# Performance work log

Hardware: AMD Instinct MI355X
Metric: run time of the kernel (lower is better)

The kernel has to match this reference:

```python
import jax, jax.numpy as jnp
import numpy as np

N = 20000
E = 320000
IN = 256
H = 4
C = 64
NEG_SLOPE = 0.2


def setup_inputs() -> dict:
    key = jax.random.key(0)
    ks = jax.random.split(key, 12)
    HC = H * C

    def w(k, shape, fan_in):
        return jax.random.normal(k, shape, dtype=jnp.float32) / np.sqrt(fan_in)

    x = jax.random.normal(ks[0], (N, IN), dtype=jnp.float32)
    edge_index = jax.random.randint(ks[1], (2, E), 0, N, dtype=jnp.int64)
    return {
        "x": x,
        "edge_index": edge_index,
        "Wl1": w(ks[2], (IN, HC), IN),
        "Wr1": w(ks[3], (IN, HC), IN),
        "att1": w(ks[4], (H, C), C),
        "b1": jnp.zeros((HC,), dtype=jnp.float32),
        "Wl2": w(ks[5], (HC, HC), HC),
        "Wr2": w(ks[6], (HC, HC), HC),
        "att2": w(ks[7], (H, C), C),
        "b2": jnp.zeros((HC,), dtype=jnp.float32),
        "Wfc": w(ks[8], (HC, 2), HC),
        "bfc": jnp.zeros((2,), dtype=jnp.float32),
    }


def _gatv2(x, src, dst, Wl, Wr, att, b):
    """GATv2Conv (concat=True, share_weights=False), inference (no dropout)."""
    n = x.shape[0]
    xl = (x @ Wl).reshape(n, H, C)  # source-side projection
    xr = (x @ Wr).reshape(n, H, C)  # target-side projection
    # per-edge GATv2 score: a^T LeakyReLU(xl_j + xr_i)
    e = jax.nn.leaky_relu(xl[src] + xr[dst], NEG_SLOPE)      # [E, H, C]
    score = jnp.einsum("ehc,hc->eh", e, att)                 # [E, H]
    # segment softmax over incoming edges of each target node
    smax = jax.ops.segment_max(score, dst, num_segments=n)   # [N, H]
    ex = jnp.exp(score - smax[dst])
    denom = jax.ops.segment_sum(ex, dst, num_segments=n)     # [N, H]
    alpha = ex / denom[dst]                                  # [E, H]
    # scatter-aggregate messages (source projections weighted by alpha)
    out = jax.ops.segment_sum(alpha[:, :, None] * xl[src], dst, num_segments=n)
    return out.reshape(n, H * C) + b


def reference(x, edge_index, Wl1, Wr1, att1, b1, Wl2, Wr2, att2, b2, Wfc, bfc):
    n = x.shape[0]
    # add_self_loops=True (PyG default)
    loop = jnp.arange(n, dtype=edge_index.dtype)
    src = jnp.concatenate([edge_index[0], loop])
    dst = jnp.concatenate([edge_index[1], loop])

    h = _gatv2(x, src, dst, Wl1, Wr1, att1, b1)
    h = jax.nn.relu(h)
    h = _gatv2(h, src, dst, Wl2, Wr2, att2, b2)
    h = jax.nn.relu(h)
    g = jnp.mean(h, axis=0, keepdims=True)  # [1, H*C]
    return g @ Wfc + bfc                    # [1, 2]
```

## Files before the change

### kernel.cpp

```cpp
#include <hip/hip_runtime.h>
#include <hip/hip_bf16.h>
#include <math.h>

#define Nn 20000
#define Ee 320000
#define INF_ 256
#define Hh 4
#define Cc 64
#define HC 256
#define NB_ 79
#define NEG_SLOPE 0.2f

using frag16 = __attribute__((ext_vector_type(8))) short;
using f32x4  = __attribute__((ext_vector_type(4))) float;

__device__ __forceinline__ void async16(const void* g, void* l) {
    __builtin_amdgcn_global_load_lds(
        (const __attribute__((address_space(1))) unsigned int*)g,
        (__attribute__((address_space(3))) unsigned int*)l,
        16, 0, 0);
}


__global__ void hist_kernel(const int* __restrict__ dst, int ne, int* deg) {
    int e = blockIdx.x * blockDim.x + threadIdx.x;
    if (e < ne) atomicAdd(&deg[dst[e]], 1);
}

#define SCAN_PER 20
__global__ __launch_bounds__(1024) void scan_all(const int* __restrict__ deg,
                                                 int* __restrict__ row_start,
                                                 int* __restrict__ cursor) {
    int tid = threadIdx.x;
    int lane = tid & 63, w = tid >> 6;
    int base = tid * SCAN_PER;
    int local[SCAN_PER];
    int sum = 0;
    #pragma unroll
    for (int i = 0; i < SCAN_PER; ++i) {
        int idx = base + i;
        int v = (idx < Nn) ? deg[idx] : 0;
        local[i] = sum;
        sum += v;
    }
    int x = sum;
    #pragma unroll
    for (int off = 1; off < 64; off <<= 1) {
        int y = __shfl_up(x, off, 64);
        if (lane >= off) x += y;
    }
    __shared__ int wsum[16];
    if (lane == 63) wsum[w] = x;
    __syncthreads();
    int wadd = 0;
    for (int k = 0; k < w; ++k) wadd += wsum[k];
    int texcl = (x - sum) + wadd;
    #pragma unroll
    for (int i = 0; i < SCAN_PER; ++i) {
        int idx = base + i;
        if (idx < Nn) {
            int v = texcl + local[i];
            row_start[idx] = v;
            cursor[idx] = v;
        }
    }
    if (tid == 1023) row_start[Nn] = texcl + sum;
}

__global__ void scatter_kernel(const int* __restrict__ src, const int* __restrict__ dst,
                               int ne, int n, int* cursor, int* colx) {
    int e = blockIdx.x * blockDim.x + threadIdx.x;
    if (e < ne) {
        int d = dst[e];
        int pos = atomicAdd(&cursor[d], 1);
        colx[pos] = src[e];
    } else if (e < ne + n) {
        int node = e - ne;
        int pos = atomicAdd(&cursor[node], 1);
        colx[pos] = node;
    }
}


__device__ inline unsigned short bf16rn(float f) {
    unsigned u = __float_as_uint(f);
    unsigned r = (u + 0x7FFFu + ((u >> 16) & 1u)) >> 16;
    return (unsigned short)r;
}

__device__ inline void split1(float v, short& h, short& l) {
    unsigned short hh = bf16rn(v);
    float back = __uint_as_float(((unsigned)hh) << 16);
    unsigned short ll = bf16rn(v - back);
    h = (short)hh; l = (short)ll;
}

__device__ __forceinline__ float4 bf4_to_f4(ushort4 u) {
    return make_float4(__uint_as_float((unsigned)u.x << 16),
                       __uint_as_float((unsigned)u.y << 16),
                       __uint_as_float((unsigned)u.z << 16),
                       __uint_as_float((unsigned)u.w << 16));
}


__global__ __launch_bounds__(256) void prep(const float* __restrict__ x,
                                            const float* __restrict__ Wl1,
                                            const float* __restrict__ Wr1,
                                            const float* __restrict__ Wl2,
                                            const float* __restrict__ Wr2,
                                            short* __restrict__ Ah,
                                            short* __restrict__ Al,
                                            short* __restrict__ WhT1,
                                            short* __restrict__ WlT1,
                                            short* __restrict__ WhT2,
                                            short* __restrict__ WlT2,
                                            int* __restrict__ deg,
                                            float* __restrict__ gpart,
                                            int n4) {
    __shared__ float T[64][65];
    int b = blockIdx.x, tid = threadIdx.x;
    if (b < 64) {
        int m  = b >> 4;
        int tr = (b >> 2) & 3;
        int tc = b & 3;
        const float* W = (m == 0) ? Wl1 : (m == 1) ? Wr1 : (m == 2) ? Wl2 : Wr2;
        short* Wh = (m < 2) ? WhT1 : WhT2;
        short* Wl = (m < 2) ? WlT1 : WlT2;
        int colofs = (m & 1) * 256;
        int lr = tid >> 4;
        int lq = (tid & 15) * 4;
        #pragma unroll
        for (int it = 0; it < 4; ++it) {
            int r = it * 16 + lr;
            float4 v = *(const float4*)&W[(size_t)(tr * 64 + r) * 256 + tc * 64 + lq];
            T[r][lq + 0] = v.x; T[r][lq + 1] = v.y;
            T[r][lq + 2] = v.z; T[r][lq + 3] = v.w;
        }
        __syncthreads();
        #pragma unroll
        for (int it = 0; it < 4; ++it) {
            int cl = it * 16 + lr;
            int kl = (tid & 15) * 4;
            short4 h, l;
            split1(T[kl + 0][cl], h.x, l.x);
            split1(T[kl + 1][cl], h.y, l.y);
            split1(T[kl + 2][cl], h.z, l.z);
            split1(T[kl + 3][cl], h.w, l.w);
            size_t o = (size_t)(colofs + tc * 64 + cl) * 256 + tr * 64 + kl;
            *(short4*)&Wh[o] = h;
            *(short4*)&Wl[o] = l;
        }
    } else {
        int i = (b - 64) * 256 + tid;
        if (i < Nn) deg[i] = 1;
        if (i < 32 * 256) gpart[i] = 0.f;
        if (i < n4) {
            float4 v = ((const float4*)x)[i];
            short4 h, l;
            split1(v.x, h.x, l.x);
            split1(v.y, h.y, l.y);
            split1(v.z, h.z, l.z);
            split1(v.w, h.w, l.w);
            ((short4*)Ah)[i] = h;
            ((short4*)Al)[i] = l;
        }
    }
}


__global__ __launch_bounds__(256, 4) void mfma_gemm(const short* __restrict__ Ah,
                                                    const short* __restrict__ Al,
                                                    const short* __restrict__ WhT,
                                                    const short* __restrict__ WlT,
                                                    unsigned short* __restrict__ XLh,
                                                    float* __restrict__ XR) {
    __shared__ short BsH[64 * 256];
    __shared__ short BsL[64 * 256];

    int tid = threadIdx.x;
    int wave = tid >> 6, lane = tid & 63;
    int quad = lane >> 4, lc = lane & 15;

    int v = blockIdx.x;
    int p = (v & 7) * 79 + (v >> 3);
    int j = p >> 3;
    int colg = p & 7;
    int cbase = (colg * 64) & 255;

    {
        int cl0 = wave * 2 + (lane >> 5);
        int kcs = (lane & 31) ^ (cl0 & 7);
        const short* srcH = WhT + (size_t)(colg * 64 + cl0) * HC + kcs * 8;
        const short* srcL = WlT + (size_t)(colg * 64 + cl0) * HC + kcs * 8;
        short* dstH = &BsH[wave * 512];
        short* dstL = &BsL[wave * 512];
        #pragma unroll
        for (int r = 0; r < 8; ++r) {
            async16(srcH + (size_t)r * 8 * HC, dstH + r * 2048);
            async16(srcL + (size_t)r * 8 * HC, dstL + r * 2048);
        }
    }
    __syncthreads();

    #pragma unroll
    for (int tt = 0; tt < 2; ++tt) {
        int rowt = j + tt * 79;
        if (rowt > 156) break;
        int bm = rowt * 128;

        int row0 = bm + wave * 32 + lc;
        int row1 = row0 + 16;
        int ca0 = (row0 < Nn) ? row0 : (Nn - 1);
        int ca1 = (row1 < Nn) ? row1 : (Nn - 1);
        const short* pa0h = Ah + (size_t)ca0 * HC + quad * 8;
        const short* pa1h = Ah + (size_t)ca1 * HC + quad * 8;
        const short* pa0l = Al + (size_t)ca0 * HC + quad * 8;
        const short* pa1l = Al + (size_t)ca1 * HC + quad * 8;

        f32x4 acc[2][4] = {};
        #pragma unroll
        for (int c = 0; c < 8; ++c) {
            int k0 = c * 32;
            frag16 a0h = *(const frag16*)(pa0h + k0);
            frag16 a1h = *(const frag16*)(pa1h + k0);
            frag16 a0l = *(const frag16*)(pa0l + k0);
            frag16 a1l = *(const frag16*)(pa1l + k0);
            int sw = ((c * 4 + quad) ^ (lc & 7)) * 8;
            frag16 bh0 = *(const frag16*)&BsH[(0 * 16 + lc) * HC + sw];
            frag16 bh1 = *(const frag16*)&BsH[(1 * 16 + lc) * HC + sw];
            frag16 bh2 = *(const frag16*)&BsH[(2 * 16 + lc) * HC + sw];
            frag16 bh3 = *(const frag16*)&BsH[(3 * 16 + lc) * HC + sw];
            frag16 bl0 = *(const frag16*)&BsL[(0 * 16 + lc) * HC + sw];
            frag16 bl1 = *(const frag16*)&BsL[(1 * 16 + lc) * HC + sw];
            frag16 bl2 = *(const frag16*)&BsL[(2 * 16 + lc) * HC + sw];
            frag16 bl3 = *(const frag16*)&BsL[(3 * 16 + lc) * HC + sw];
            acc[0][0] = __builtin_amdgcn_mfma_f32_16x16x32_bf16(bh0, a0h, acc[0][0], 0, 0, 0);
            acc[1][0] = __builtin_amdgcn_mfma_f32_16x16x32_bf16(bh0, a1h, acc[1][0], 0, 0, 0);
            acc[0][1] = __builtin_amdgcn_mfma_f32_16x16x32_bf16(bh1, a0h, acc[0][1], 0, 0, 0);
            acc[1][1] = __builtin_amdgcn_mfma_f32_16x16x32_bf16(bh1, a1h, acc[1][1], 0, 0, 0);
            acc[0][2] = __builtin_amdgcn_mfma_f32_16x16x32_bf16(bh2, a0h, acc[0][2], 0, 0, 0);
            acc[1][2] = __builtin_amdgcn_mfma_f32_16x16x32_bf16(bh2, a1h, acc[1][2], 0, 0, 0);
            acc[0][3] = __builtin_amdgcn_mfma_f32_16x16x32_bf16(bh3, a0h, acc[0][3], 0, 0, 0);
            acc[1][3] = __builtin_amdgcn_mfma_f32_16x16x32_bf16(bh3, a1h, acc[1][3], 0, 0, 0);
            acc[0][0] = __builtin_amdgcn_mfma_f32_16x16x32_bf16(bh0, a0l, acc[0][0], 0, 0, 0);
            acc[1][0] = __builtin_amdgcn_mfma_f32_16x16x32_bf16(bh0, a1l, acc[1][0], 0, 0, 0);
            acc[0][1] = __builtin_amdgcn_mfma_f32_16x16x32_bf16(bh1, a0l, acc[0][1], 0, 0, 0);
            acc[1][1] = __builtin_amdgcn_mfma_f32_16x16x32_bf16(bh1, a1l, acc[1][1], 0, 0, 0);
            acc[0][2] = __builtin_amdgcn_mfma_f32_16x16x32_bf16(bh2, a0l, acc[0][2], 0, 0, 0);
            acc[1][2] = __builtin_amdgcn_mfma_f32_16x16x32_bf16(bh2, a1l, acc[1][2], 0, 0, 0);
            acc[0][3] = __builtin_amdgcn_mfma_f32_16x16x32_bf16(bh3, a0l, acc[0][3], 0, 0, 0);
            acc[1][3] = __builtin_amdgcn_mfma_f32_16x16x32_bf16(bh3, a1l, acc[1][3], 0, 0, 0);
            acc[0][0] = __builtin_amdgcn_mfma_f32_16x16x32_bf16(bl0, a0h, acc[0][0], 0, 0, 0);
            acc[1][0] = __builtin_amdgcn_mfma_f32_16x16x32_bf16(bl0, a1h, acc[1][0], 0, 0, 0);
            acc[0][1] = __builtin_amdgcn_mfma_f32_16x16x32_bf16(bl1, a0h, acc[0][1], 0, 0, 0);
            acc[1][1] = __builtin_amdgcn_mfma_f32_16x16x32_bf16(bl1, a1h, acc[1][1], 0, 0, 0);
            acc[0][2] = __builtin_amdgcn_mfma_f32_16x16x32_bf16(bl2, a0h, acc[0][2], 0, 0, 0);
            acc[1][2] = __builtin_amdgcn_mfma_f32_16x16x32_bf16(bl2, a1h, acc[1][2], 0, 0, 0);
            acc[0][3] = __builtin_amdgcn_mfma_f32_16x16x32_bf16(bl3, a0h, acc[0][3], 0, 0, 0);
            acc[1][3] = __builtin_amdgcn_mfma_f32_16x16x32_bf16(bl3, a1h, acc[1][3], 0, 0, 0);
        }

        #pragma unroll
        for (int mt = 0; mt < 2; ++mt) {
            int rw = bm + wave * 32 + mt * 16 + lc;
            if (rw >= Nn) continue;
            #pragma unroll
            for (int t = 0; t < 4; ++t) {
                int col0 = cbase + t * 16 + quad * 4;
                if (colg < 4) {
                    ushort4 o;
                    o.x = bf16rn(acc[mt][t][0]);
                    o.y = bf16rn(acc[mt][t][1]);
                    o.z = bf16rn(acc[mt][t][2]);
                    o.w = bf16rn(acc[mt][t][3]);
                    *(ushort4*)&XLh[(size_t)rw * HC + col0] = o;
                } else {
                    *(f32x4*)&XR[(size_t)rw * HC + col0] = acc[mt][t];
                }
            }
        }
    }
}


__device__ __forceinline__ float edge_score(const float4 v, const float4 xr,
                                            const float4 a06, const float4 a04) {
    float tx = v.x + xr.x, ty = v.y + xr.y, tz = v.z + xr.z, tw = v.w + xr.w;
    float p = a06.x * tx + a04.x * fabsf(tx);
    p += a06.y * ty + a04.y * fabsf(ty);
    p += a06.z * tz + a04.z * fabsf(tz);
    p += a06.w * tw + a04.w * fabsf(tw);
    p += __shfl_xor(p, 1, 64);
    p += __shfl_xor(p, 2, 64);
    p += __shfl_xor(p, 4, 64);
    p += __shfl_xor(p, 8, 64);
    return p;
}

__global__ __launch_bounds__(256) void gat_kernel(const ushort4* __restrict__ XL4,
                                                  const float4* __restrict__ XR4,
                                                  const int* __restrict__ row_start,
                                                  const int* __restrict__ colx,
                                                  const float4* __restrict__ att4,
                                                  const float4* __restrict__ bias4,
                                                  float* __restrict__ gpart,
                                                  short4* __restrict__ Ahi,
                                                  short4* __restrict__ Alo,
                                                  int mode) {
    __shared__ float4 sred[4][64];
    int wave = threadIdx.x >> 6, lane = threadIdx.x & 63;
    int node = blockIdx.x * 4 + wave;
    float4 xr = XR4[(size_t)node * 64 + lane];
    float4 a  = att4[lane];
    float4 a06 = make_float4(a.x * 0.6f, a.y * 0.6f, a.z * 0.6f, a.w * 0.6f);
    float4 a04 = make_float4(a.x * 0.4f, a.y * 0.4f, a.z * 0.4f, a.w * 0.4f);
    int e0 = __builtin_amdgcn_readfirstlane(row_start[node]);
    int e1 = __builtin_amdgcn_readfirstlane(row_start[node + 1]);
    float l0 = 0.f, l1 = 0.f;
    float4 acc0 = make_float4(0.f, 0.f, 0.f, 0.f);
    float4 acc1 = make_float4(0.f, 0.f, 0.f, 0.f);
    int npairs = (e1 - e0) >> 1;
    int e = e0;
    ushort4 u0 = make_ushort4(0, 0, 0, 0), u1 = u0;
    int na = 0, nb = 0;
    if (npairs > 0) {
        int sa = colx[e0], sb = colx[e0 + 1];
        u0 = XL4[(size_t)sa * 64 + lane];
        u1 = XL4[(size_t)sb * 64 + lane];
        if (npairs > 1) { na = colx[e0 + 2]; nb = colx[e0 + 3]; }
        else            { na = sa; nb = sb; }
    }
    for (int pp = 0; pp < npairs; ++pp) {
        int en = e + 2;
        ushort4 nu0 = XL4[(size_t)na * 64 + lane];
        ushort4 nu1 = XL4[(size_t)nb * 64 + lane];
        bool more2 = (pp + 2 < npairs);
        int f0 = more2 ? en + 2 : e;
        int f1 = more2 ? en + 3 : e;
        int ta = colx[f0], tb = colx[f1];
        float4 v0 = bf4_to_f4(u0);
        float4 v1 = bf4_to_f4(u1);
        float pe0 = __expf(edge_score(v0, xr, a06, a04));
        float pe1 = __expf(edge_score(v1, xr, a06, a04));
        l0 += pe0; l1 += pe1;
        acc0.x += pe0 * v0.x; acc0.y += pe0 * v0.y;
        acc0.z += pe0 * v0.z; acc0.w += pe0 * v0.w;
        acc1.x += pe1 * v1.x; acc1.y += pe1 * v1.y;
        acc1.z += pe1 * v1.z; acc1.w += pe1 * v1.w;
        u0 = nu0; u1 = nu1; na = ta; nb = tb; e = en;
    }
    if (e < e1) {
        int st = colx[e];
        float4 v0 = bf4_to_f4(XL4[(size_t)st * 64 + lane]);
        float pe0 = __expf(edge_score(v0, xr, a06, a04));
        l0 += pe0;
        acc0.x += pe0 * v0.x; acc0.y += pe0 * v0.y;
        acc0.z += pe0 * v0.z; acc0.w += pe0 * v0.w;
    }
    float rl = 1.f / (l0 + l1);
    float4 b = bias4[lane];
    float4 o = make_float4(fmaxf((acc0.x + acc1.x) * rl + b.x, 0.f),
                           fmaxf((acc0.y + acc1.y) * rl + b.y, 0.f),
                           fmaxf((acc0.z + acc1.z) * rl + b.z, 0.f),
                           fmaxf((acc0.w + acc1.w) * rl + b.w, 0.f));
    if (mode) {
        short4 h4, l4;
        split1(o.x, h4.x, l4.x);
        split1(o.y, h4.y, l4.y);
        split1(o.z, h4.z, l4.z);
        split1(o.w, h4.w, l4.w);
        size_t oidx = (size_t)node * 64 + lane;
        Ahi[oidx] = h4;
        Alo[oidx] = l4;
    } else {
        sred[wave][lane] = o;
        __syncthreads();
        if (threadIdx.x < 64) {
            int l = threadIdx.x;
            float4 s = sred[0][l];
            float4 s1v = sred[1][l], s2v = sred[2][l], s3v = sred[3][l];
            s.x += s1v.x + s2v.x + s3v.x;
            s.y += s1v.y + s2v.y + s3v.y;
            s.z += s1v.z + s2v.z + s3v.z;
            s.w += s1v.w + s2v.w + s3v.w;
            float* gp = gpart + (blockIdx.x & 31) * 256 + l * 4;
            atomicAdd(gp + 0, s.x);
            atomicAdd(gp + 1, s.y);
            atomicAdd(gp + 2, s.z);
            atomicAdd(gp + 3, s.w);
        }
    }
}


__global__ __launch_bounds__(256) void fc_kernel(const float* __restrict__ gpart,
                                                 const float* __restrict__ Wfc,
                                                 const float* __restrict__ bfc,
                                                 float* __restrict__ out, float invN) {
    int t = threadIdx.x;
    float s = 0.f;
    #pragma unroll
    for (int k = 0; k < 32; ++k) s += gpart[k * 256 + t];
    float gv = s * invN;
    float p0 = gv * Wfc[2 * t];
    float p1 = gv * Wfc[2 * t + 1];
    #pragma unroll
    for (int off = 32; off > 0; off >>= 1) {
        p0 += __shfl_xor(p0, off, 64);
        p1 += __shfl_xor(p1, off, 64);
    }
    __shared__ float s0[4], s1[4];
    if ((t & 63) == 0) { s0[t >> 6] = p0; s1[t >> 6] = p1; }
    __syncthreads();
    if (t == 0) {
        out[0] = s0[0] + s0[1] + s0[2] + s0[3] + bfc[0];
        out[1] = s1[0] + s1[1] + s1[2] + s1[3] + bfc[1];
    }
}


extern "C" void kernel_launch(void* const* d_in, const int* in_sizes, int n_in,
                              void* d_out, int out_size, void* d_ws, size_t ws_size,
                              hipStream_t stream) {
    const float* x    = (const float*)d_in[0];
    const int*   eidx = (const int*)d_in[1];
    const float* Wl1  = (const float*)d_in[2];
    const float* Wr1  = (const float*)d_in[3];
    const float* att1 = (const float*)d_in[4];
    const float* b1   = (const float*)d_in[5];
    const float* Wl2  = (const float*)d_in[6];
    const float* Wr2  = (const float*)d_in[7];
    const float* att2 = (const float*)d_in[8];
    const float* b2   = (const float*)d_in[9];
    const float* Wfc  = (const float*)d_in[10];
    const float* bfc  = (const float*)d_in[11];
    float* out = (float*)d_out;

    const int* srcv = eidx;
    const int* dstv = eidx + Ee;

    size_t NHC = (size_t)Nn * HC;
    float* XR = (float*)d_ws;
    float* gpart = XR + NHC;
    unsigned short* XLh = (unsigned short*)(gpart + 32 * 256);
    short* Ah   = (short*)(XLh + NHC);
    short* Al   = Ah + NHC;
    short* WhT1 = Al + NHC;
    short* WlT1 = WhT1 + 512 * 256;
    short* WhT2 = WlT1 + 512 * 256;
    short* WlT2 = WhT2 + 512 * 256;
    int* deg       = (int*)(WlT2 + 512 * 256);
    int* row_start = deg + Nn;
    int* cursor    = row_start + (Nn + 1);
    int* colx      = cursor + Nn;

    const int N4 = (int)(NHC / 4);

    prep<<<64 + (N4 + 255) / 256, 256, 0, stream>>>(x, Wl1, Wr1, Wl2, Wr2,
                                                    Ah, Al, WhT1, WlT1, WhT2, WlT2,
                                                    deg, gpart, N4);

    hist_kernel<<<(Ee + 255) / 256, 256, 0, stream>>>(dstv, Ee, deg);
    scan_all<<<1, 1024, 0, stream>>>(deg, row_start, cursor);
    scatter_kernel<<<(Ee + Nn + 255) / 256, 256, 0, stream>>>(srcv, dstv, Ee, Nn, cursor, colx);

    const int GB = 8 * 79;

    mfma_gemm<<<GB, 256, 0, stream>>>(Ah, Al, WhT1, WlT1, XLh, XR);
    gat_kernel<<<Nn / 4, 256, 0, stream>>>((const ushort4*)XLh, (const float4*)XR,
                                           row_start, colx, (const float4*)att1,
                                           (const float4*)b1, gpart,
                                           (short4*)Ah, (short4*)Al, 1);

    mfma_gemm<<<GB, 256, 0, stream>>>(Ah, Al, WhT2, WlT2, XLh, XR);
    gat_kernel<<<Nn / 4, 256, 0, stream>>>((const ushort4*)XLh, (const float4*)XR,
                                           row_start, colx, (const float4*)att2,
                                           (const float4*)b2, gpart,
                                           (short4*)Ah, (short4*)Al, 0);

    fc_kernel<<<1, 256, 0, stream>>>(gpart, Wfc, bfc, out, 1.0f / Nn);
}
```

Baseline: 271.9 us.

## Use one row tile per GEMM block, read low weights from global, simplify gather prefetch

```diff
diff --git a/kernel.cpp b/kernel.cpp
--- a/kernel.cpp
+++ b/kernel.cpp
@@ -175,108 +175,99 @@
                                                     unsigned short* __restrict__ XLh,
                                                     float* __restrict__ XR) {
     __shared__ short BsH[64 * 256];
-    __shared__ short BsL[64 * 256];
 
     int tid = threadIdx.x;
     int wave = tid >> 6, lane = tid & 63;
     int quad = lane >> 4, lc = lane & 15;
 
     int v = blockIdx.x;
-    int p = (v & 7) * 79 + (v >> 3);
-    int j = p >> 3;
+    int p = (v & 7) * 157 + (v >> 3);
+    int rowt = p >> 3;
     int colg = p & 7;
+    int bm = rowt * 128;
     int cbase = (colg * 64) & 255;
 
     {
         int cl0 = wave * 2 + (lane >> 5);
         int kcs = (lane & 31) ^ (cl0 & 7);
         const short* srcH = WhT + (size_t)(colg * 64 + cl0) * HC + kcs * 8;
-        const short* srcL = WlT + (size_t)(colg * 64 + cl0) * HC + kcs * 8;
         short* dstH = &BsH[wave * 512];
-        short* dstL = &BsL[wave * 512];
         #pragma unroll
-        for (int r = 0; r < 8; ++r) {
+        for (int r = 0; r < 8; ++r)
             async16(srcH + (size_t)r * 8 * HC, dstH + r * 2048);
-            async16(srcL + (size_t)r * 8 * HC, dstL + r * 2048);
-        }
-    }
+    }
+
+    int row0 = bm + wave * 32 + lc;
+    int row1 = row0 + 16;
+    int ca0 = (row0 < Nn) ? row0 : (Nn - 1);
+    int ca1 = (row1 < Nn) ? row1 : (Nn - 1);
+    const short* pa0h = Ah + (size_t)ca0 * HC + quad * 8;
+    const short* pa1h = Ah + (size_t)ca1 * HC + quad * 8;
+    const short* pa0l = Al + (size_t)ca0 * HC + quad * 8;
+    const short* pa1l = Al + (size_t)ca1 * HC + quad * 8;
+    const short* pbl = WlT + (size_t)(colg * 64 + lc) * HC + quad * 8;
+
     __syncthreads();
 
-    #pragma unroll
-    for (int tt = 0; tt < 2; ++tt) {
-        int rowt = j + tt * 79;
-        if (rowt > 156) break;
-        int bm = rowt * 128;
-
-        int row0 = bm + wave * 32 + lc;
-        int row1 = row0 + 16;
-        int ca0 = (row0 < Nn) ? row0 : (Nn - 1);
-        int ca1 = (row1 < Nn) ? row1 : (Nn - 1);
-        const short* pa0h = Ah + (size_t)ca0 * HC + quad * 8;
-        const short* pa1h = Ah + (size_t)ca1 * HC + quad * 8;
-        const short* pa0l = Al + (size_t)ca0 * HC + quad * 8;
-        const short* pa1l = Al + (size_t)ca1 * HC + quad * 8;
-
-        f32x4 acc[2][4] = {};
+    f32x4 acc[2][4] = {};
+    #pragma unroll
+    for (int c = 0; c < 8; ++c) {
+        int k0 = c * 32;
+        frag16 a0h = *(const frag16*)(pa0h + k0);
+        frag16 a1h = *(const frag16*)(pa1h + k0);
+        frag16 a0l = *(const frag16*)(pa0l + k0);
+        frag16 a1l = *(const frag16*)(pa1l + k0);
+        int sw = ((c * 4 + quad) ^ (lc & 7)) * 8;
+        frag16 bh0 = *(const frag16*)&BsH[(0 * 16 + lc) * HC + sw];
+        frag16 bh1 = *(const frag16*)&BsH[(1 * 16 + lc) * HC + sw];
+        frag16 bh2 = *(const frag16*)&BsH[(2 * 16 + lc) * HC + sw];
+        frag16 bh3 = *(const frag16*)&BsH[(3 * 16 + lc) * HC + sw];
+        frag16 bl0 = *(const frag16*)(pbl + (size_t)0 * 16 * HC + k0);
+        frag16 bl1 = *(const frag16*)(pbl + (size_t)1 * 16 * HC + k0);
+        frag16 bl2 = *(const frag16*)(pbl + (size_t)2 * 16 * HC + k0);
+        frag16 bl3 = *(const frag16*)(pbl + (size_t)3 * 16 * HC + k0);
+        acc[0][0] = __builtin_amdgcn_mfma_f32_16x16x32_bf16(bh0, a0h, acc[0][0], 0, 0, 0);
+        acc[1][0] = __builtin_amdgcn_mfma_f32_16x16x32_bf16(bh0, a1h, acc[1][0], 0, 0, 0);
+        acc[0][1] = __builtin_amdgcn_mfma_f32_16x16x32_bf16(bh1, a0h, acc[0][1], 0, 0, 0);
+        acc[1][1] = __builtin_amdgcn_mfma_f32_16x16x32_bf16(bh1, a1h, acc[1][1], 0, 0, 0);
+        acc[0][2] = __builtin_amdgcn_mfma_f32_16x16x32_bf16(bh2, a0h, acc[0][2], 0, 0, 0);
+        acc[1][2] = __builtin_amdgcn_mfma_f32_16x16x32_bf16(bh2, a1h, acc[1][2], 0, 0, 0);
+        acc[0][3] = __builtin_amdgcn_mfma_f32_16x16x32_bf16(bh3, a0h, acc[0][3], 0, 0, 0);
+        acc[1][3] = __builtin_amdgcn_mfma_f32_16x16x32_bf16(bh3, a1h, acc[1][3], 0, 0, 0);
+        acc[0][0] = __builtin_amdgcn_mfma_f32_16x16x32_bf16(bh0, a0l, acc[0][0], 0, 0, 0);
+        acc[1][0] = __builtin_amdgcn_mfma_f32_16x16x32_bf16(bh0, a1l, acc[1][0], 0, 0, 0);
+        acc[0][1] = __builtin_amdgcn_mfma_f32_16x16x32_bf16(bh1, a0l, acc[0][1], 0, 0, 0);
+        acc[1][1] = __builtin_amdgcn_mfma_f32_16x16x32_bf16(bh1, a1l, acc[1][1], 0, 0, 0);
+        acc[0][2] = __builtin_amdgcn_mfma_f32_16x16x32_bf16(bh2, a0l, acc[0][2], 0, 0, 0);
+        acc[1][2] = __builtin_amdgcn_mfma_f32_16x16x32_bf16(bh2, a1l, acc[1][2], 0, 0, 0);
+        acc[0][3] = __builtin_amdgcn_mfma_f32_16x16x32_bf16(bh3, a0l, acc[0][3], 0, 0, 0);
+        acc[1][3] = __builtin_amdgcn_mfma_f32_16x16x32_bf16(bh3, a1l, acc[1][3], 0, 0, 0);
+        acc[0][0] = __builtin_amdgcn_mfma_f32_16x16x32_bf16(bl0, a0h, acc[0][0], 0, 0, 0);
+        acc[1][0] = __builtin_amdgcn_mfma_f32_16x16x32_bf16(bl0, a1h, acc[1][0], 0, 0, 0);
+        acc[0][1] = __builtin_amdgcn_mfma_f32_16x16x32_bf16(bl1, a0h, acc[0][1], 0, 0, 0);
+        acc[1][1] = __builtin_amdgcn_mfma_f32_16x16x32_bf16(bl1, a1h, acc[1][1], 0, 0, 0);
+        acc[0][2] = __builtin_amdgcn_mfma_f32_16x16x32_bf16(bl2, a0h, acc[0][2], 0, 0, 0);
+        acc[1][2] = __builtin_amdgcn_mfma_f32_16x16x32_bf16(bl2, a1h, acc[1][2], 0, 0, 0);
+        acc[0][3] = __builtin_amdgcn_mfma_f32_16x16x32_bf16(bl3, a0h, acc[0][3], 0, 0, 0);
+        acc[1][3] = __builtin_amdgcn_mfma_f32_16x16x32_bf16(bl3, a1h, acc[1][3], 0, 0, 0);
+    }
+
+    #pragma unroll
+    for (int mt = 0; mt < 2; ++mt) {
+        int rw = bm + wave * 32 + mt * 16 + lc;
+        if (rw >= Nn) continue;
         #pragma unroll
-        for (int c = 0; c < 8; ++c) {
-            int k0 = c * 32;
-            frag16 a0h = *(const frag16*)(pa0h + k0);
-            frag16 a1h = *(const frag16*)(pa1h + k0);
-            frag16 a0l = *(const frag16*)(pa0l + k0);
-            frag16 a1l = *(const frag16*)(pa1l + k0);
-            int sw = ((c * 4 + quad) ^ (lc & 7)) * 8;
-            frag16 bh0 = *(const frag16*)&BsH[(0 * 16 + lc) * HC + sw];
-            frag16 bh1 = *(const frag16*)&BsH[(1 * 16 + lc) * HC + sw];
-            frag16 bh2 = *(const frag16*)&BsH[(2 * 16 + lc) * HC + sw];
-            frag16 bh3 = *(const frag16*)&BsH[(3 * 16 + lc) * HC + sw];
-            frag16 bl0 = *(const frag16*)&BsL[(0 * 16 + lc) * HC + sw];
-            frag16 bl1 = *(const frag16*)&BsL[(1 * 16 + lc) * HC + sw];
-            frag16 bl2 = *(const frag16*)&BsL[(2 * 16 + lc) * HC + sw];
-            frag16 bl3 = *(const frag16*)&BsL[(3 * 16 + lc) * HC + sw];
-            acc[0][0] = __builtin_amdgcn_mfma_f32_16x16x32_bf16(bh0, a0h, acc[0][0], 0, 0, 0);
-            acc[1][0] = __builtin_amdgcn_mfma_f32_16x16x32_bf16(bh0, a1h, acc[1][0], 0, 0, 0);
-            acc[0][1] = __builtin_amdgcn_mfma_f32_16x16x32_bf16(bh1, a0h, acc[0][1], 0, 0, 0);
-            acc[1][1] = __builtin_amdgcn_mfma_f32_16x16x32_bf16(bh1, a1h, acc[1][1], 0, 0, 0);
-            acc[0][2] = __builtin_amdgcn_mfma_f32_16x16x32_bf16(bh2, a0h, acc[0][2], 0, 0, 0);
-            acc[1][2] = __builtin_amdgcn_mfma_f32_16x16x32_bf16(bh2, a1h, acc[1][2], 0, 0, 0);
-            acc[0][3] = __builtin_amdgcn_mfma_f32_16x16x32_bf16(bh3, a0h, acc[0][3], 0, 0, 0);
-            acc[1][3] = __builtin_amdgcn_mfma_f32_16x16x32_bf16(bh3, a1h, acc[1][3], 0, 0, 0);
-            acc[0][0] = __builtin_amdgcn_mfma_f32_16x16x32_bf16(bh0, a0l, acc[0][0], 0, 0, 0);
-            acc[1][0] = __builtin_amdgcn_mfma_f32_16x16x32_bf16(bh0, a1l, acc[1][0], 0, 0, 0);
-            acc[0][1] = __builtin_amdgcn_mfma_f32_16x16x32_bf16(bh1, a0l, acc[0][1], 0, 0, 0);
-            acc[1][1] = __builtin_amdgcn_mfma_f32_16x16x32_bf16(bh1, a1l, acc[1][1], 0, 0, 0);
-            acc[0][2] = __builtin_amdgcn_mfma_f32_16x16x32_bf16(bh2, a0l, acc[0][2], 0, 0, 0);
-            acc[1][2] = __builtin_amdgcn_mfma_f32_16x16x32_bf16(bh2, a1l, acc[1][2], 0, 0, 0);
-            acc[0][3] = __builtin_amdgcn_mfma_f32_16x16x32_bf16(bh3, a0l, acc[0][3], 0, 0, 0);
-            acc[1][3] = __builtin_amdgcn_mfma_f32_16x16x32_bf16(bh3, a1l, acc[1][3], 0, 0, 0);
-            acc[0][0] = __builtin_amdgcn_mfma_f32_16x16x32_bf16(bl0, a0h, acc[0][0], 0, 0, 0);
-            acc[1][0] = __builtin_amdgcn_mfma_f32_16x16x32_bf16(bl0, a1h, acc[1][0], 0, 0, 0);
-            acc[0][1] = __builtin_amdgcn_mfma_f32_16x16x32_bf16(bl1, a0h, acc[0][1], 0, 0, 0);
-            acc[1][1] = __builtin_amdgcn_mfma_f32_16x16x32_bf16(bl1, a1h, acc[1][1], 0, 0, 0);
-            acc[0][2] = __builtin_amdgcn_mfma_f32_16x16x32_bf16(bl2, a0h, acc[0][2], 0, 0, 0);
-            acc[1][2] = __builtin_amdgcn_mfma_f32_16x16x32_bf16(bl2, a1h, acc[1][2], 0, 0, 0);
-            acc[0][3] = __builtin_amdgcn_mfma_f32_16x16x32_bf16(bl3, a0h, acc[0][3], 0, 0, 0);
-            acc[1][3] = __builtin_amdgcn_mfma_f32_16x16x32_bf16(bl3, a1h, acc[1][3], 0, 0, 0);
-        }
-
-        #pragma unroll
-        for (int mt = 0; mt < 2; ++mt) {
-            int rw = bm + wave * 32 + mt * 16 + lc;
-            if (rw >= Nn) continue;
-            #pragma unroll
-            for (int t = 0; t < 4; ++t) {
-                int col0 = cbase + t * 16 + quad * 4;
-                if (colg < 4) {
-                    ushort4 o;
-                    o.x = bf16rn(acc[mt][t][0]);
-                    o.y = bf16rn(acc[mt][t][1]);
-                    o.z = bf16rn(acc[mt][t][2]);
-                    o.w = bf16rn(acc[mt][t][3]);
-                    *(ushort4*)&XLh[(size_t)rw * HC + col0] = o;
-                } else {
-                    *(f32x4*)&XR[(size_t)rw * HC + col0] = acc[mt][t];
-                }
+        for (int t = 0; t < 4; ++t) {
+            int col0 = cbase + t * 16 + quad * 4;
+            if (colg < 4) {
+                ushort4 o;
+                o.x = bf16rn(acc[mt][t][0]);
+                o.y = bf16rn(acc[mt][t][1]);
+                o.z = bf16rn(acc[mt][t][2]);
+                o.w = bf16rn(acc[mt][t][3]);
+                *(ushort4*)&XLh[(size_t)rw * HC + col0] = o;
+            } else {
+                *(f32x4*)&XR[(size_t)rw * HC + col0] = acc[mt][t];
             }
         }
     }
@@ -321,23 +312,16 @@
     float4 acc1 = make_float4(0.f, 0.f, 0.f, 0.f);
     int npairs = (e1 - e0) >> 1;
     int e = e0;
-    ushort4 u0 = make_ushort4(0, 0, 0, 0), u1 = u0;
-    int na = 0, nb = 0;
-    if (npairs > 0) {
-        int sa = colx[e0], sb = colx[e0 + 1];
-        u0 = XL4[(size_t)sa * 64 + lane];
-        u1 = XL4[(size_t)sb * 64 + lane];
-        if (npairs > 1) { na = colx[e0 + 2]; nb = colx[e0 + 3]; }
-        else            { na = sa; nb = sb; }
-    }
+    int s0 = 0, s1 = 0;
+    if (npairs > 0) { s0 = colx[e]; s1 = colx[e + 1]; }
     for (int pp = 0; pp < npairs; ++pp) {
         int en = e + 2;
-        ushort4 nu0 = XL4[(size_t)na * 64 + lane];
-        ushort4 nu1 = XL4[(size_t)nb * 64 + lane];
-        bool more2 = (pp + 2 < npairs);
-        int f0 = more2 ? en + 2 : e;
-        int f1 = more2 ? en + 3 : e;
-        int ta = colx[f0], tb = colx[f1];
+        int i0 = (en     < e1) ? en     : (e1 - 1);
+        int i1 = (en + 1 < e1) ? en + 1 : (e1 - 1);
+        int ns0 = colx[i0];
+        int ns1 = colx[i1];
+        ushort4 u0 = XL4[(size_t)s0 * 64 + lane];
+        ushort4 u1 = XL4[(size_t)s1 * 64 + lane];
         float4 v0 = bf4_to_f4(u0);
         float4 v1 = bf4_to_f4(u1);
         float pe0 = __expf(edge_score(v0, xr, a06, a04));
@@ -347,7 +331,7 @@
         acc0.z += pe0 * v0.z; acc0.w += pe0 * v0.w;
         acc1.x += pe1 * v1.x; acc1.y += pe1 * v1.y;
         acc1.z += pe1 * v1.z; acc1.w += pe1 * v1.w;
-        u0 = nu0; u1 = nu1; na = ta; nb = tb; e = en;
+        s0 = ns0; s1 = ns1; e = en;
     }
     if (e < e1) {
         int st = colx[e];
@@ -464,7 +448,7 @@
     scan_all<<<1, 1024, 0, stream>>>(deg, row_start, cursor);
     scatter_kernel<<<(Ee + Nn + 255) / 256, 256, 0, stream>>>(srcv, dstv, Ee, Nn, cursor, colx);
 
-    const int GB = 8 * 79;
+    const int GB = 8 * 157;
 
     mfma_gemm<<<GB, 256, 0, stream>>>(Ah, Al, WhT1, WlT1, XLh, XR);
     gat_kernel<<<Nn / 4, 256, 0, stream>>>((const ushort4*)XLh, (const float4*)XR,
```

Measured after the change: 304.2 us. 1.12x slower.
